# Kernel optimization log

Measured on AMD Instinct MI355X. Metric: run time of the kernel, lower is better.

Reference implementation:

```python
import jax, jax.numpy as jnp
import numpy as np

HEADS = 20  # head_dim = 1280 // 20 = 64
LORA_SCALE = 1.0


def setup_inputs() -> dict:
    key = jax.random.key(0)
    ks = jax.random.split(key, 16)
    B, S, C, R = 2, 2048, 1280, 4
    w = 0.02  # keep activations numerically tame
    inp = {
        "x": jax.random.normal(ks[0], (B, S, C), jnp.float32),
        "Wq": jax.random.normal(ks[1], (C, C), jnp.float32) * w,
        "Wk": jax.random.normal(ks[2], (C, C), jnp.float32) * w,
        "Wv": jax.random.normal(ks[3], (C, C), jnp.float32) * w,
        "Wo": jax.random.normal(ks[4], (C, C), jnp.float32) * w,
        "bo": jnp.zeros((C,), jnp.float32),
        "Aq": jax.random.normal(ks[5], (R, C), jnp.float32) * w,
        "Bq": jax.random.normal(ks[6], (C, R), jnp.float32) * w,
        "Ak": jax.random.normal(ks[7], (R, C), jnp.float32) * w,
        "Bk": jax.random.normal(ks[8], (C, R), jnp.float32) * w,
        "Av": jax.random.normal(ks[9], (R, C), jnp.float32) * w,
        "Bv": jax.random.normal(ks[10], (C, R), jnp.float32) * w,
        "Ao": jax.random.normal(ks[11], (R, C), jnp.float32) * w,
        "Bo": jax.random.normal(ks[12], (C, R), jnp.float32) * w,
    }
    return inp


def _lora(x, A, B):
    # LoRALinearLayer: up(down(x)); network_alpha=None -> no extra scaling
    return (x @ A.T) @ B.T


def reference(x, Wq, Wk, Wv, Wo, bo, Aq, Bq, Ak, Bk, Av, Bv, Ao, Bo):
    B, S, C = x.shape
    H = HEADS
    D = C // H
    # base projections + LoRA updates (self-attention: encoder_hidden_states = x)
    q = x @ Wq.T + LORA_SCALE * _lora(x, Aq, Bq)
    k = x @ Wk.T + LORA_SCALE * _lora(x, Ak, Bk)
    v = x @ Wv.T + LORA_SCALE * _lora(x, Av, Bv)
    # head split: [B, S, H, D]
    q = q.reshape(B, S, H, D)
    k = k.reshape(B, S, H, D)
    v = v.reshape(B, S, H, D)
    # explicit scores + softmax (attn.get_attention_scores), scale = 1/sqrt(D)
    scale = 1.0 / jnp.sqrt(jnp.asarray(D, x.dtype))
    scores = jnp.einsum("bshd,bthd->bhst", q, k) * scale  # [B, H, S, S]
    probs = jax.nn.softmax(scores, axis=-1)
    ctx = jnp.einsum("bhst,bthd->bshd", probs, v).reshape(B, S, C)
    # output projection (+bias) + LoRA; dropout is identity at eval
    out = ctx @ Wo.T + bo + LORA_SCALE * _lora(ctx, Ao, Bo)
    return out
```

## Files before the change

### kernel.cpp

```cpp
#include <hip/hip_runtime.h>

#define BATCH 2
#define SEQ   2048
#define CH    1280
#define NH    20
#define HD    64
#define BS    (BATCH*SEQ)
#define RK    4

typedef __attribute__((ext_vector_type(2)))  float floatx2;
typedef __attribute__((ext_vector_type(4)))  short bf16x4;
typedef __attribute__((ext_vector_type(8)))  short bf16x8;
typedef __attribute__((ext_vector_type(16))) float floatx16;

__device__ __forceinline__ floatx16 mfma32(bf16x8 a, bf16x8 b, floatx16 c) {
    return __builtin_amdgcn_mfma_f32_32x32x16_bf16(a, b, c, 0, 0, 0);
}
__device__ __forceinline__ floatx16 mfma32k8(bf16x4 a, bf16x4 b, floatx16 c) {
    return __builtin_amdgcn_mfma_f32_32x32x8bf16_1k(a, b, c, 0, 0, 0);
}

__device__ __forceinline__ unsigned short f2bf(float f) {
    unsigned int u = __float_as_uint(f);
    u += 0x7fffu + ((u >> 16) & 1u);
    return (unsigned short)(u >> 16);
}
__device__ __forceinline__ unsigned int packbf(float hi, float lo) {
    unsigned int a = __float_as_uint(hi) + 0x8000u;
    unsigned int b = __float_as_uint(lo) + 0x8000u;
    return __builtin_amdgcn_perm(a, b, 0x07060302u);
}
__device__ __forceinline__ float fexp2(float x) {
#if __has_builtin(__builtin_amdgcn_exp2f)
    return __builtin_amdgcn_exp2f(x);
#else
    return exp2f(x);
#endif
}

__device__ __forceinline__ void cp16(const unsigned short* g, unsigned short* l) {
    __builtin_amdgcn_global_load_lds(
        (const __attribute__((address_space(1))) unsigned int*)g,
        (__attribute__((address_space(3))) unsigned int*)l, 16, 0, 0);
}

#define F4_BLOCKS   (CH * CH / 1024)
#define CAST_BLOCKS (BS * CH / 1024)

__global__ __launch_bounds__(256) void prep(
    const float* __restrict__ x,
    const float* __restrict__ Wq, const float* __restrict__ Wk,
    const float* __restrict__ Wv, const float* __restrict__ Wo,
    const float* __restrict__ Aq, const float* __restrict__ Bq,
    const float* __restrict__ Ak, const float* __restrict__ Bk,
    const float* __restrict__ Av, const float* __restrict__ Bv,
    const float* __restrict__ Ao, const float* __restrict__ Bo,
    unsigned short* __restrict__ wq_bf, unsigned short* __restrict__ wk_bf,
    unsigned short* __restrict__ wv_bf, unsigned short* __restrict__ wo_bf,
    unsigned short* __restrict__ xb)
{
    const int bx = blockIdx.x;
    if (bx < 4 * F4_BLOCKS) {
        int which = bx / F4_BLOCKS;
        int e = ((bx % F4_BLOCKS) * 256 + threadIdx.x) * 4;
        int i = e / CH, j = e % CH;
        const float *W, *A, *Bm;
        unsigned short* o;
        if (which == 0)      { W = Wq; A = Aq; Bm = Bq; o = wq_bf; }
        else if (which == 1) { W = Wk; A = Ak; Bm = Bk; o = wk_bf; }
        else if (which == 2) { W = Wv; A = Av; Bm = Bv; o = wv_bf; }
        else                 { W = Wo; A = Ao; Bm = Bo; o = wo_bf; }
        float4 acc = *(const float4*)(W + e);
#pragma unroll
        for (int r = 0; r < RK; r++) {
            float bm = Bm[i * RK + r];
            float4 a4 = *(const float4*)(A + r * CH + j);
            acc.x += bm * a4.x; acc.y += bm * a4.y;
            acc.z += bm * a4.z; acc.w += bm * a4.w;
        }
        ushort4 ov;
        ov.x = f2bf(acc.x); ov.y = f2bf(acc.y);
        ov.z = f2bf(acc.z); ov.w = f2bf(acc.w);
        *(ushort4*)(o + e) = ov;
    } else {
        int idx = ((bx - 4 * F4_BLOCKS) * 256 + threadIdx.x) * 4;
        float4 v = *(const float4*)(x + idx);
        ushort4 o;
        o.x = f2bf(v.x); o.y = f2bf(v.y); o.z = f2bf(v.z); o.w = f2bf(v.w);
        *(ushort4*)(xb + idx) = o;
    }
}

__device__ __forceinline__ void gemm128(
    const unsigned short* __restrict__ A, const unsigned short* __restrict__ B,
    unsigned short* __restrict__ obf, float* __restrict__ of,
    const float* __restrict__ bias, float oscale, int mode,
    unsigned short* __restrict__ vt)
{
    __shared__ __align__(16) unsigned short smem[2 * 128 * 64];
    unsigned short* sa = smem;
    unsigned short* sb = smem + 128 * 64;
    const int tid = threadIdx.x;
    const int wav = tid >> 6, lane = tid & 63;
    const int n32 = lane & 31, half = lane >> 5;
    const int wr = wav >> 1, wc = wav & 1;
    const int M0 = blockIdx.y * 128, N0 = blockIdx.x * 128;

    const unsigned short* ga[4]; const unsigned short* gb[4];
    unsigned short* la[4]; unsigned short* lb[4];
#pragma unroll
    for (int g = 0; g < 4; g++) {
        int s = g * 256 + tid;
        int row = s >> 3, cc = (s & 7) ^ (row & 7);
        ga[g] = A + (size_t)(M0 + row) * CH + cc * 8;
        gb[g] = B + (size_t)(N0 + row) * CH + cc * 8;
        la[g] = sa + (size_t)(g * 256 + wav * 64) * 8;
        lb[g] = sb + (size_t)(g * 256 + wav * 64) * 8;
    }

    const int arow0 = wr * 64 + n32, brow0 = wc * 64 + n32;

    floatx16 acc[2][2];
#pragma unroll
    for (int mt = 0; mt < 2; mt++)
#pragma unroll
        for (int nt = 0; nt < 2; nt++)
#pragma unroll
            for (int r = 0; r < 16; r++) acc[mt][nt][r] = 0.f;

    for (int k0 = 0; k0 < CH; k0 += 64) {
#pragma unroll
        for (int g = 0; g < 4; g++) { cp16(ga[g], la[g]); cp16(gb[g], lb[g]); }
#pragma unroll
        for (int g = 0; g < 4; g++) { ga[g] += 64; gb[g] += 64; }
        __syncthreads();

        bf16x8 av[2][4], bv[2][4];
#pragma unroll
        for (int mt = 0; mt < 2; mt++) {
            const int ar = arow0 + mt * 32, br = brow0 + mt * 32;
#pragma unroll
            for (int ks = 0; ks < 4; ks++) {
                const int cc = ks * 2 + half;
                av[mt][ks] = *(const bf16x8*)(sa + ar * 64 + ((cc ^ (ar & 7)) << 3));
                bv[mt][ks] = *(const bf16x8*)(sb + br * 64 + ((cc ^ (br & 7)) << 3));
            }
        }
#pragma unroll
        for (int ks = 0; ks < 4; ks++)
#pragma unroll
            for (int mt = 0; mt < 2; mt++)
#pragma unroll
                for (int nt = 0; nt < 2; nt++)
                    acc[mt][nt] = mfma32(av[mt][ks], bv[nt][ks], acc[mt][nt]);
        __syncthreads();
    }

    if (mode == 2) {
#pragma unroll
        for (int mt = 0; mt < 2; mt++) {
#pragma unroll
            for (int nt = 0; nt < 2; nt++) {
                const int dl = wc * 64 + nt * 32 + n32;
#pragma unroll
                for (int j = 0; j < 4; j++) {
                    const int u = wr * 16 + mt * 8 + 2 * j + half;
                    uint2 w;
                    w.x = packbf(acc[mt][nt][4 * j + 1], acc[mt][nt][4 * j + 0]);
                    w.y = packbf(acc[mt][nt][4 * j + 3], acc[mt][nt][4 * j + 2]);
                    *(uint2*)(smem + dl * 128 + ((u ^ n32) << 2)) = w;
                }
            }
        }
        __syncthreads();
        const int b = M0 >> 11;
        const int s_in = M0 & (SEQ - 1);
#pragma unroll
        for (int g = 0; g < 8; g++) {
            int cid = g * 256 + tid;
            int dl = cid >> 4, pc = cid & 15;
            int g32 = pc >> 2, p = (pc & 3) >> 1, hb = pc & 1;
            int u1 = 8 * g32 + 4 * p + hb;
            int sw = dl & 31;
            uint2 r1 = *(const uint2*)(smem + dl * 128 + ((u1 ^ sw) << 2));
            uint2 r2 = *(const uint2*)(smem + dl * 128 + (((u1 + 2) ^ sw) << 2));
            int ch = N0 + dl, h = ch >> 6, d = ch & 63;
            uint4 val; val.x = r1.x; val.y = r1.y; val.z = r2.x; val.w = r2.y;
            *(uint4*)(vt + (size_t)((b * NH + h) * HD + d) * SEQ + s_in + pc * 8) = val;
        }
        return;
    }

#pragma unroll
    for (int mt = 0; mt < 2; mt++) {
#pragma unroll
        for (int nt = 0; nt < 2; nt++) {
            const int col = N0 + wc * 64 + nt * 32 + n32;
            const float bv2 = (mode == 1) ? bias[col] : 0.f;
#pragma unroll
            for (int r = 0; r < 16; r++) {
                size_t row = (size_t)(M0 + wr * 64 + mt * 32 +
                                      (r & 3) + 8 * (r >> 2) + 4 * half);
                if (mode == 1) of[row * CH + col] = acc[mt][nt][r] + bv2;
                else           obf[row * CH + col] = f2bf(acc[mt][nt][r] * oscale);
            }
        }
    }
}

__global__ __launch_bounds__(256) void gemm_qkv(
    const unsigned short* __restrict__ xb,
    const unsigned short* __restrict__ wq, const unsigned short* __restrict__ wk,
    const unsigned short* __restrict__ wv,
    unsigned short* __restrict__ q, unsigned short* __restrict__ k,
    unsigned short* __restrict__ vt)
{
    const unsigned short* w = blockIdx.z == 0 ? wq : blockIdx.z == 1 ? wk : wv;
    unsigned short* o = blockIdx.z == 0 ? q : k;
    float scale = blockIdx.z == 0 ? 0.18033688011112042f : 1.0f;
    int mode = blockIdx.z == 2 ? 2 : 0;
    gemm128(xb, w, o, nullptr, nullptr, scale, mode, vt);
}

__global__ __launch_bounds__(256) void gemm_o(
    const unsigned short* __restrict__ c_bf, const unsigned short* __restrict__ wo,
    const float* __restrict__ bias, float* __restrict__ out)
{
    gemm128(c_bf, wo, nullptr, out, bias, 1.0f, 1, nullptr);
}

__global__ __launch_bounds__(512, 4) void attention(
    const unsigned short* __restrict__ q, const unsigned short* __restrict__ k,
    const unsigned short* __restrict__ vt, unsigned short* __restrict__ c_bf)
{
    __shared__ __align__(16) unsigned short smem[128 * 64 + 64 * 128];
    unsigned short* k_lds = smem;
    unsigned short* v_lds = smem + 128 * 64;

    const int tid = threadIdx.x, wav = tid >> 6, lane = tid & 63;
    const int n32 = lane & 31, half = lane >> 5;
    const int qg = wav >> 1, kh = wav & 1;
    const int q0 = blockIdx.x * 128;
    const int bh = blockIdx.y, b = bh / NH, h = bh % NH;

    const size_t qrow = (size_t)(b * SEQ + q0 + qg * 32 + n32);
    bf16x8 qf[4];
#pragma unroll
    for (int f = 0; f < 4; f++)
        qf[f] = *(const bf16x8*)(q + qrow * CH + h * HD + f * 16 + half * 8);

    const int rowk = tid >> 3, cck = (tid & 7) ^ (rowk & 7);
    const int rowv = tid >> 4, ccv = (tid & 15) ^ (rowv & 15);
    const unsigned short* gk0 = k + (size_t)(b * SEQ + rowk) * CH + h * HD + cck * 8;
    const unsigned short* gv0 = vt + (size_t)(bh * HD + rowv) * SEQ + ccv * 8;
    unsigned short* lk0 = k_lds + (size_t)(wav * 64) * 8;
    unsigned short* lv0 = v_lds + (size_t)(wav * 64) * 8;

    floatx2 ps = {0.f, 0.f};
    floatx16 acc[2];
#pragma unroll
    for (int dt = 0; dt < 2; dt++)
#pragma unroll
        for (int r = 0; r < 16; r++) acc[dt][r] = 0.f;

    for (int t0 = 0; t0 < SEQ; t0 += 128) {
#pragma unroll
        for (int g = 0; g < 2; g++) {
            cp16(gk0 + (size_t)g * 64 * CH, lk0 + g * 4096);
            cp16(gv0 + (size_t)g * 32 * SEQ, lv0 + g * 4096);
        }
        gk0 += (size_t)128 * CH; gv0 += 128;
        __syncthreads();

#pragma unroll
        for (int ktl = 0; ktl < 2; ktl++) {
            const int kt = kh * 2 + ktl;
            const int keyrow = kt * 32 + n32;
            const unsigned short* kr = k_lds + keyrow * 64;
            floatx16 st;
#pragma unroll
            for (int r = 0; r < 16; r++) st[r] = 0.f;
#pragma unroll
            for (int f = 0; f < 4; f++) {
                int phys = (2 * f + half) ^ (keyrow & 7);
                bf16x8 kf = *(const bf16x8*)(kr + phys * 8);
                st = mfma32(kf, qf[f], st);
            }

#pragma unroll
            for (int pp = 0; pp < 2; pp++) {
                float p[8];
#pragma unroll
                for (int r = 0; r < 8; r++) p[r] = fexp2(st[8 * pp + r]);
                unsigned int pk[4];
#pragma unroll
                for (int j = 0; j < 4; j++) {
                    ps += (floatx2){p[2 * j], p[2 * j + 1]};
                    pk[j] = packbf(p[2 * j + 1], p[2 * j]);
                }
                union { unsigned int u[2]; bf16x4 v; } pb0, pb1;
                pb0.u[0] = pk[0]; pb0.u[1] = pk[1];
                pb1.u[0] = pk[2]; pb1.u[1] = pk[3];
#pragma unroll
                for (int dt = 0; dt < 2; dt++) {
                    const int drow = dt * 32 + n32;
                    int ct = kt * 4 + pp * 2 + half;
                    int phys = ct ^ (drow & 15);
                    union { bf16x8 v8; bf16x4 v4[2]; } vv;
                    vv.v8 = *(const bf16x8*)(v_lds + drow * 128 + phys * 8);
                    acc[dt] = mfma32k8(vv.v4[0], pb0.v, acc[dt]);
                    acc[dt] = mfma32k8(vv.v4[1], pb1.v, acc[dt]);
                }
            }
        }
        __syncthreads();
    }

    float psum = ps.x + ps.y;
    float* ex = (float*)smem;
#pragma unroll
    for (int p2 = 0; p2 < 2; p2++) {
        __syncthreads();
        if (kh == 1 && (qg >> 1) == p2) {
            float* dst = ex + (size_t)((qg & 1) * 64 + lane) * 33;
#pragma unroll
            for (int dt = 0; dt < 2; dt++)
#pragma unroll
                for (int r = 0; r < 16; r++) dst[dt * 16 + r] = acc[dt][r];
            dst[32] = psum;
        }
        __syncthreads();
        if (kh == 0 && (qg >> 1) == p2) {
            const float* src = ex + (size_t)((qg & 1) * 64 + lane) * 33;
#pragma unroll
            for (int dt = 0; dt < 2; dt++)
#pragma unroll
                for (int r = 0; r < 16; r++) acc[dt][r] += src[dt * 16 + r];
            psum += src[32];
        }
    }
    if (kh) return;

    float tot = psum + __shfl_xor(psum, 32, 64);
    float rinv = __frcp_rn(tot);
    const size_t obase = qrow * CH + h * HD;
#pragma unroll
    for (int dt = 0; dt < 2; dt++) {
#pragma unroll
        for (int jj = 0; jj < 4; jj++) {
            int d = dt * 32 + 8 * jj + 4 * half;
            uint2 o2;
            o2.x = packbf(acc[dt][4 * jj + 1] * rinv, acc[dt][4 * jj + 0] * rinv);
            o2.y = packbf(acc[dt][4 * jj + 3] * rinv, acc[dt][4 * jj + 2] * rinv);
            *(uint2*)(c_bf + obase + d) = o2;
        }
    }
}

extern "C" void kernel_launch(void* const* d_in, const int* in_sizes, int n_in,
                              void* d_out, int out_size, void* d_ws, size_t ws_size,
                              hipStream_t stream)
{
    const float* x  = (const float*)d_in[0];
    const float* Wq = (const float*)d_in[1];
    const float* Wk = (const float*)d_in[2];
    const float* Wv = (const float*)d_in[3];
    const float* Wo = (const float*)d_in[4];
    const float* bo = (const float*)d_in[5];
    const float* Aq = (const float*)d_in[6];
    const float* Bq = (const float*)d_in[7];
    const float* Ak = (const float*)d_in[8];
    const float* Bk = (const float*)d_in[9];
    const float* Av = (const float*)d_in[10];
    const float* Bv = (const float*)d_in[11];
    const float* Ao = (const float*)d_in[12];
    const float* Bo = (const float*)d_in[13];
    float* out = (float*)d_out;

    char* ws = (char*)d_ws;
    size_t off = 0;
    auto alloc = [&](size_t bytes) -> void* {
        void* p = ws + off; off += (bytes + 255) & ~(size_t)255; return p;
    };
    const size_t WB = (size_t)CH * CH, XB = (size_t)BS * CH;
    unsigned short* wq_bf = (unsigned short*)alloc(WB * 2);
    unsigned short* wk_bf = (unsigned short*)alloc(WB * 2);
    unsigned short* wv_bf = (unsigned short*)alloc(WB * 2);
    unsigned short* wo_bf = (unsigned short*)alloc(WB * 2);
    unsigned short* x_bf  = (unsigned short*)alloc(XB * 2);
    unsigned short* q_bf  = (unsigned short*)alloc(XB * 2);
    unsigned short* k_bf  = (unsigned short*)alloc(XB * 2);
    unsigned short* vt_bf = (unsigned short*)alloc(XB * 2);
    unsigned short* c_bf  = (unsigned short*)alloc(XB * 2);
    (void)ws_size; (void)n_in; (void)in_sizes; (void)out_size;

    prep<<<dim3(4 * F4_BLOCKS + CAST_BLOCKS), 256, 0, stream>>>(
        x, Wq, Wk, Wv, Wo, Aq, Bq, Ak, Bk, Av, Bv, Ao, Bo,
        wq_bf, wk_bf, wv_bf, wo_bf, x_bf);

    gemm_qkv<<<dim3(CH / 128, BS / 128, 3), 256, 0, stream>>>(
        x_bf, wq_bf, wk_bf, wv_bf, q_bf, k_bf, vt_bf);

    attention<<<dim3(SEQ / 128, BATCH * NH), 512, 0, stream>>>(
        q_bf, k_bf, vt_bf, c_bf);

    gemm_o<<<dim3(CH / 128, BS / 128), 256, 0, stream>>>(c_bf, wo_bf, bo, out);
}
```

Before: 262.2 us.

## Double-buffer K/V tiles in attention to overlap global loads with compute

Doubles the attention kernel's LDS allocation into two K/V buffers. The next tile is prefetched with async copies while the current one is computed, using explicit vmcnt waits and barriers in place of the load-then-sync loop. This is meant to hide global-to-LDS latency behind the MFMA work. LDS use doubles to 64KB per block, which may reduce occupancy relative to the launch bound of 4 blocks, and correctness relies on the hand-set vmcnt(4) matching the number of outstanding copies.

```diff
diff --git a/kernel.cpp b/kernel.cpp
--- a/kernel.cpp
+++ b/kernel.cpp
@@ -233,9 +233,7 @@
     const unsigned short* __restrict__ q, const unsigned short* __restrict__ k,
     const unsigned short* __restrict__ vt, unsigned short* __restrict__ c_bf)
 {
-    __shared__ __align__(16) unsigned short smem[128 * 64 + 64 * 128];
-    unsigned short* k_lds = smem;
-    unsigned short* v_lds = smem + 128 * 64;
+    __shared__ __align__(16) unsigned short smem[2 * (128 * 64 + 64 * 128)];
 
     const int tid = threadIdx.x, wav = tid >> 6, lane = tid & 63;
     const int n32 = lane & 31, half = lane >> 5;
@@ -253,8 +251,18 @@
     const int rowv = tid >> 4, ccv = (tid & 15) ^ (rowv & 15);
     const unsigned short* gk0 = k + (size_t)(b * SEQ + rowk) * CH + h * HD + cck * 8;
     const unsigned short* gv0 = vt + (size_t)(bh * HD + rowv) * SEQ + ccv * 8;
-    unsigned short* lk0 = k_lds + (size_t)(wav * 64) * 8;
-    unsigned short* lv0 = v_lds + (size_t)(wav * 64) * 8;
+
+    auto STAGE = [&](int t, int bufb) {
+        const unsigned short* gk = gk0 + (size_t)t * 128 * CH;
+        const unsigned short* gv = gv0 + t * 128;
+        unsigned short* lk = smem + bufb * 16384 + wav * 512;
+        unsigned short* lv = smem + bufb * 16384 + 8192 + wav * 512;
+#pragma unroll
+        for (int g = 0; g < 2; g++) {
+            cp16(gk + (size_t)g * 64 * CH, lk + g * 4096);
+            cp16(gv + (size_t)g * 32 * SEQ, lv + g * 4096);
+        }
+    };
 
     floatx2 ps = {0.f, 0.f};
     floatx16 acc[2];
@@ -263,15 +271,9 @@
 #pragma unroll
         for (int r = 0; r < 16; r++) acc[dt][r] = 0.f;
 
-    for (int t0 = 0; t0 < SEQ; t0 += 128) {
-#pragma unroll
-        for (int g = 0; g < 2; g++) {
-            cp16(gk0 + (size_t)g * 64 * CH, lk0 + g * 4096);
-            cp16(gv0 + (size_t)g * 32 * SEQ, lv0 + g * 4096);
-        }
-        gk0 += (size_t)128 * CH; gv0 += 128;
-        __syncthreads();
-
+    auto COMPUTE = [&](int bufb) {
+        const unsigned short* k_lds = smem + bufb * 16384;
+        const unsigned short* v_lds = k_lds + 8192;
 #pragma unroll
         for (int ktl = 0; ktl < 2; ktl++) {
             const int kt = kh * 2 + ktl;
@@ -313,8 +315,21 @@
                 }
             }
         }
-        __syncthreads();
-    }
+    };
+
+    STAGE(0, 0);
+    for (int it = 0; it < 15; it++) {
+        STAGE(it + 1, (it + 1) & 1);
+        asm volatile("s_waitcnt vmcnt(4)" ::: "memory");
+        __builtin_amdgcn_s_barrier();
+        __builtin_amdgcn_sched_barrier(0);
+        COMPUTE(it & 1);
+        __builtin_amdgcn_s_barrier();
+    }
+    asm volatile("s_waitcnt vmcnt(0)" ::: "memory");
+    __builtin_amdgcn_s_barrier();
+    __builtin_amdgcn_sched_barrier(0);
+    COMPUTE(1);
 
     float psum = ps.x + ps.y;
     float* ex = (float*)smem;
```

After: 260.8 us. About the same (-0.5%).
